# Optimization experiments

Measured on AMD Instinct MI355X. Metric: run time of the kernel, lower is better.

Reference implementation:

```python
import jax, jax.numpy as jnp
import numpy as np

N_NODES = 100000
N_EDGES = 1600000
IN_FEATS = 128
N_HIDDEN = 128
OUT_DIM = 32
BN_EPS = 1e-5


def setup_inputs() -> dict:
    key = jax.random.key(0)
    ks = jax.random.split(key, 12)
    s = 0.05  # weight init scale
    return {
        "features": jax.random.normal(ks[0], (N_NODES, IN_FEATS), dtype=jnp.float32),
        "src": jax.random.randint(ks[1], (N_EDGES,), 0, N_NODES),
        "dst": jax.random.randint(ks[2], (N_EDGES,), 0, N_NODES),
        # layer 0: in_feats -> n_hidden
        "Ws0": jax.random.normal(ks[3], (IN_FEATS, N_HIDDEN), dtype=jnp.float32) * s,
        "Wn0": jax.random.normal(ks[4], (IN_FEATS, N_HIDDEN), dtype=jnp.float32) * s,
        "b0": jnp.zeros((N_HIDDEN,), jnp.float32),
        # layer 1: n_hidden -> n_hidden
        "Ws1": jax.random.normal(ks[5], (N_HIDDEN, N_HIDDEN), dtype=jnp.float32) * s,
        "Wn1": jax.random.normal(ks[6], (N_HIDDEN, N_HIDDEN), dtype=jnp.float32) * s,
        "b1": jnp.zeros((N_HIDDEN,), jnp.float32),
        # layer 2 (output): n_hidden -> out_dim, no activation
        "Ws2": jax.random.normal(ks[7], (N_HIDDEN, OUT_DIM), dtype=jnp.float32) * s,
        "Wn2": jax.random.normal(ks[8], (N_HIDDEN, OUT_DIM), dtype=jnp.float32) * s,
        "b2": jnp.zeros((OUT_DIM,), jnp.float32),
        # batch norms after layers 0 and 1
        "g0": jnp.ones((N_HIDDEN,), jnp.float32),
        "be0": jnp.zeros((N_HIDDEN,), jnp.float32),
        "g1": jnp.ones((N_HIDDEN,), jnp.float32),
        "be1": jnp.zeros((N_HIDDEN,), jnp.float32),
    }


def _sage_mean(h, src, dst, inv_deg, Ws, Wn, b):
    # DGL SAGEConv('mean'): fc_self(h) + fc_neigh(mean of in-neighbor feats)
    agg = jax.ops.segment_sum(h[src], dst, num_segments=N_NODES) * inv_deg
    return h @ Ws + agg @ Wn + b


def _batch_norm(h, gamma, beta):
    mu = jnp.mean(h, axis=0)
    var = jnp.var(h, axis=0)
    return (h - mu) * jax.lax.rsqrt(var + BN_EPS) * gamma + beta


def reference(features, src, dst, Ws0, Wn0, b0, Ws1, Wn1, b1, Ws2, Wn2, b2, g0, be0, g1, be1):
    ones = jnp.ones((N_EDGES,), jnp.float32)
    deg = jax.ops.segment_sum(ones, dst, num_segments=N_NODES)
    inv_deg = (1.0 / jnp.maximum(deg, 1.0))[:, None]  # [N,1]

    # layer 0: SAGEConv internal activation, then BN + external activation
    h = jax.nn.relu(_sage_mean(features, src, dst, inv_deg, Ws0, Wn0, b0))
    h = jax.nn.relu(_batch_norm(h, g0, be0))
    # layer 1 (hidden)
    h = jax.nn.relu(_sage_mean(h, src, dst, inv_deg, Ws1, Wn1, b1))
    h = jax.nn.relu(_batch_norm(h, g1, be1))
    # layer 2 (output): no activation, no BN (idx > n_hidden_layers)
    h = _sage_mean(h, src, dst, inv_deg, Ws2, Wn2, b2)

    # dgl.mean_nodes over a single graph -> [1, out_dim], then softmax over classes
    hg = jnp.mean(h, axis=0, keepdims=True)
    return jax.nn.softmax(hg, axis=1)
```

## Files before the change

kernel.cpp:

```cpp
#include <hip/hip_runtime.h>
#include <hip/hip_bf16.h>

typedef __hip_bfloat16 bf16;
typedef __hip_bfloat162 bf162;

#define NN 100000
#define NE 1600000
#define BN_EPS 1e-5f

#define BSH 8
#define NBUCK ((NN + 255) >> BSH)
#define ABLK 128
#define EPBA ((NE + ABLK - 1) / ABLK)
#define CAP 6144

struct alignas(16) bf16x8 { bf16 v[8]; };

typedef __bf16 bfrag __attribute__((ext_vector_type(8)));
typedef float f4 __attribute__((ext_vector_type(4)));
typedef float f2 __attribute__((ext_vector_type(2)));

static __device__ __forceinline__ float b2f(bf16 x){ return __bfloat162float(x); }
static __device__ __forceinline__ bf16 f2b(float x){ return __float2bfloat16(x); }

static __device__ __forceinline__ uint2 pk8_fp8(float x0,float x1,float x2,float x3,
                                                float x4,float x5,float x6,float x7)
{
    int lo = __builtin_amdgcn_cvt_pk_fp8_f32(x0, x1, 0, 0);
    lo = __builtin_amdgcn_cvt_pk_fp8_f32(x2, x3, lo, 1);
    int hi = __builtin_amdgcn_cvt_pk_fp8_f32(x4, x5, 0, 0);
    hi = __builtin_amdgcn_cvt_pk_fp8_f32(x6, x7, hi, 1);
    return make_uint2((unsigned)lo, (unsigned)hi);
}

__global__ __launch_bounds__(256) void k_convert(const float* __restrict__ in,
                                                 unsigned char* __restrict__ outf8, int n)
{
    int i = (blockIdx.x * 256 + threadIdx.x) * 8;
    if (i + 7 < n) {
        float4 a = *(const float4*)(in + i);
        float4 b = *(const float4*)(in + i + 4);
        *(uint2*)(outf8 + i) = pk8_fp8(a.x,a.y,a.z,a.w,b.x,b.y,b.z,b.w);
    }
}

__global__ __launch_bounds__(256) void k_wtrans(const float* __restrict__ W0, const float* __restrict__ W1,
                                                const float* __restrict__ W2, const float* __restrict__ W3,
                                                bf16* __restrict__ T0, bf16* __restrict__ T1,
                                                bf16* __restrict__ T2, bf16* __restrict__ T3)
{
    int m = blockIdx.x >> 6;
    int t = (blockIdx.x & 63) * 256 + threadIdx.x;
    const float* W = (m == 0) ? W0 : (m == 1) ? W1 : (m == 2) ? W2 : W3;
    bf16* T = (m == 0) ? T0 : (m == 1) ? T1 : (m == 2) ? T2 : T3;
    int n = t >> 7, k = t & 127;
    T[n * 128 + k] = f2b(W[k * 128 + n]);
}

__global__ __launch_bounds__(256) void k_pa1(const int* __restrict__ dst, const int* __restrict__ src,
                                             int* __restrict__ bucketCountD, int* __restrict__ blockBaseD,
                                             int* __restrict__ bucketCountS, int* __restrict__ blockBaseS)
{
    __shared__ int histD[NBUCK];
    __shared__ int histS[NBUCK];
    int t = threadIdx.x;
    for (int i = t; i < NBUCK; i += 256) { histD[i] = 0; histS[i] = 0; }
    __syncthreads();
    int e0 = blockIdx.x * EPBA, e1 = min(e0 + EPBA, NE);
    for (int e = e0 + t; e < e1; e += 256) {
        unsigned bd = ((unsigned)dst[e]) >> BSH;
        unsigned bs = ((unsigned)src[e]) >> BSH;
        if (bd < (unsigned)NBUCK) atomicAdd(&histD[bd], 1);
        if (bs < (unsigned)NBUCK) atomicAdd(&histS[bs], 1);
    }
    __syncthreads();
    for (int i = t; i < NBUCK; i += 256) {
        blockBaseD[blockIdx.x * NBUCK + i] = atomicAdd(&bucketCountD[i], histD[i]);
        blockBaseS[blockIdx.x * NBUCK + i] = atomicAdd(&bucketCountS[i], histS[i]);
    }
}

__global__ __launch_bounds__(512) void k_bscan2(const int* __restrict__ cntD, int* __restrict__ startD,
                                                const int* __restrict__ cntS, int* __restrict__ startS)
{
    __shared__ int sd[512];
    const int* cnt = (blockIdx.x == 0) ? cntD : cntS;
    int* start = (blockIdx.x == 0) ? startD : startS;
    int t = threadIdx.x;
    int v = (t < NBUCK) ? cnt[t] : 0;
    sd[t] = v;
    __syncthreads();
    for (int o = 1; o < 512; o <<= 1) {
        int x = (t >= o) ? sd[t - o] : 0;
        __syncthreads();
        sd[t] += x;
        __syncthreads();
    }
    if (t < NBUCK) start[t] = sd[t] - v;
    if (t == 0) start[NBUCK] = NE;
}

__global__ __launch_bounds__(256) void k_pa2(const int* __restrict__ src, const int* __restrict__ dst,
                                             const int* __restrict__ bucketStartD, const int* __restrict__ blockBaseD,
                                             const int* __restrict__ bucketStartS, const int* __restrict__ blockBaseS,
                                             unsigned* __restrict__ packD, unsigned* __restrict__ packS)
{
    __shared__ int baseD[NBUCK];
    __shared__ int curD[NBUCK];
    __shared__ int baseS[NBUCK];
    __shared__ int curS[NBUCK];
    int t = threadIdx.x;
    for (int i = t; i < NBUCK; i += 256) {
        baseD[i] = bucketStartD[i] + blockBaseD[blockIdx.x * NBUCK + i];
        curD[i] = 0;
        baseS[i] = bucketStartS[i] + blockBaseS[blockIdx.x * NBUCK + i];
        curS[i] = 0;
    }
    __syncthreads();
    int e0 = blockIdx.x * EPBA, e1 = min(e0 + EPBA, NE);
    for (int e = e0 + t; e < e1; e += 256) {
        int s = src[e], d = dst[e];
        unsigned bd = ((unsigned)d) >> BSH;
        if (bd < (unsigned)NBUCK) {
            int r = atomicAdd(&curD[bd], 1);
            unsigned idx = (unsigned)(baseD[bd] + r);
            if (idx < (unsigned)NE)
                packD[idx] = (((unsigned)d & 255u) << 24) | ((unsigned)s & 0xFFFFFFu);
        }
        unsigned bs = ((unsigned)s) >> BSH;
        if (bs < (unsigned)NBUCK) {
            int r = atomicAdd(&curS[bs], 1);
            unsigned idx = (unsigned)(baseS[bs] + r);
            if (idx < (unsigned)NE)
                packS[idx] = (((unsigned)s & 255u) << 24) | ((unsigned)d & 0xFFFFFFu);
        }
    }
}

__global__ __launch_bounds__(256) void k_pbD(const unsigned* __restrict__ packD, const int* __restrict__ bucketStartD,
                                             int* __restrict__ offs, float* __restrict__ invd,
                                             int* __restrict__ esrc)
{
    __shared__ int dcnt[256];
    __shared__ int sscan[256];
    __shared__ int cur[256];
    __shared__ int S[CAP];
    int t = threadIdx.x;
    int b = blockIdx.x;
    int base = b << BSH;
    dcnt[t] = 0;
    cur[t] = 0;
    for (int i = t; i < CAP; i += 256) S[i] = 0;
    __syncthreads();
    int p0 = bucketStartD[b], p1 = bucketStartD[b + 1];
    int cnt = p1 - p0;
    for (int i = p0 + t; i < p1; i += 256)
        atomicAdd(&dcnt[packD[i] >> 24], 1);
    __syncthreads();
    int my = dcnt[t];
    sscan[t] = my;
    __syncthreads();
    for (int o = 1; o < 256; o <<= 1) {
        int v = (t >= o) ? sscan[t - o] : 0;
        __syncthreads();
        sscan[t] += v;
        __syncthreads();
    }
    int lo = sscan[t] - my;
    if (base + t < NN) {
        offs[base + t] = p0 + lo;
        invd[base + t] = 1.0f / (float)max(my, 1);
    }
    if (b == NBUCK - 1 && t == 0) offs[NN] = NE;
    __syncthreads();
    sscan[t] = lo;
    __syncthreads();
    if (cnt <= CAP) {
        for (int i = p0 + t; i < p1; i += 256) {
            unsigned v = packD[i];
            unsigned li = v >> 24;
            int pos = sscan[li] + atomicAdd(&cur[li], 1);
            if ((unsigned)pos >= (unsigned)cnt) pos = cnt - 1;
            S[pos] = (int)(v & 0xFFFFFFu);
        }
        __syncthreads();
        for (int i = t; i < cnt; i += 256) esrc[p0 + i] = S[i];
    } else {
        for (int i = p0 + t; i < p1; i += 256) {
            unsigned v = packD[i];
            unsigned li = v >> 24;
            int pos = sscan[li] + atomicAdd(&cur[li], 1);
            if ((unsigned)pos >= (unsigned)cnt) pos = cnt - 1;
            esrc[p0 + pos] = (int)(v & 0xFFFFFFu);
        }
    }
}

__global__ __launch_bounds__(256) void k_wsrc2(const unsigned* __restrict__ packS, const int* __restrict__ bucketStartS,
                                               const float* __restrict__ invd, float* __restrict__ wsrc)
{
    __shared__ float wacc[256];
    int t = threadIdx.x;
    wacc[t] = 0.f;
    __syncthreads();
    int b = blockIdx.x;
    int base = b << BSH;
    int p0 = bucketStartS[b], p1 = bucketStartS[b + 1];
    for (int i = p0 + t; i < p1; i += 256) {
        unsigned v = packS[i];
        unsigned li = v >> 24;
        unsigned dy = v & 0xFFFFFFu;
        if (dy >= (unsigned)NN) dy = 0u;
        atomicAdd(&wacc[li], invd[dy]);
    }
    __syncthreads();
    if (base + t < NN) wsrc[base + t] = wacc[t];
}

__global__ __launch_bounds__(256) void k_aggregate(const unsigned char* __restrict__ inf8, bf16* __restrict__ out,
                                                   const int* __restrict__ offs, const int* __restrict__ esrc,
                                                   const float* __restrict__ invd,
                                                   const float* __restrict__ scsh, int use_ss)
{
    int row = blockIdx.x * 4 + (threadIdx.x >> 6);
    if (row >= NN) return;
    int lane = threadIdx.x & 63;
    int grp = lane >> 4;
    int c0 = (lane & 15) * 8;
    float sc[8], sh[8];
    if (use_ss) {
#pragma unroll
        for (int j = 0; j < 8; j++) { sc[j] = scsh[c0 + j]; sh[j] = scsh[128 + c0 + j]; }
    }
    int e0 = offs[row], e1 = offs[row + 1];
    float a[8];
#pragma unroll
    for (int j = 0; j < 8; j++) a[j] = 0.f;

    auto unpack = [&](uint2 u, float* v) {
        f2 p0 = __builtin_amdgcn_cvt_pk_f32_fp8(u.x, 0);
        f2 p1 = __builtin_amdgcn_cvt_pk_f32_fp8(u.x, 1);
        f2 p2 = __builtin_amdgcn_cvt_pk_f32_fp8(u.y, 0);
        f2 p3 = __builtin_amdgcn_cvt_pk_f32_fp8(u.y, 1);
        v[0]=p0.x; v[1]=p0.y; v[2]=p1.x; v[3]=p1.y; v[4]=p2.x; v[5]=p2.y; v[6]=p3.x; v[7]=p3.y;
    };

    int e = e0 + grp;
    for (; e + 12 < e1; e += 16) {
        int s0 = esrc[e], s1 = esrc[e + 4], s2 = esrc[e + 8], s3 = esrc[e + 12];
        uint2 u0 = *(const uint2*)&inf8[(size_t)s0 * 128 + c0];
        uint2 u1 = *(const uint2*)&inf8[(size_t)s1 * 128 + c0];
        uint2 u2 = *(const uint2*)&inf8[(size_t)s2 * 128 + c0];
        uint2 u3 = *(const uint2*)&inf8[(size_t)s3 * 128 + c0];
        float v0[8], v1[8], v2[8], v3[8];
        unpack(u0, v0); unpack(u1, v1); unpack(u2, v2); unpack(u3, v3);
        if (use_ss) {
#pragma unroll
            for (int j = 0; j < 8; j++)
                a[j] += fmaxf(v0[j] * sc[j] + sh[j], 0.f) + fmaxf(v1[j] * sc[j] + sh[j], 0.f)
                      + fmaxf(v2[j] * sc[j] + sh[j], 0.f) + fmaxf(v3[j] * sc[j] + sh[j], 0.f);
        } else {
#pragma unroll
            for (int j = 0; j < 8; j++)
                a[j] += (v0[j] + v1[j]) + (v2[j] + v3[j]);
        }
    }
    if (e < e1) {
        int i1 = e + 4, i2 = e + 8;
        float m1 = (i1 < e1) ? 1.f : 0.f;
        float m2 = (i2 < e1) ? 1.f : 0.f;
        if (i1 >= e1) i1 = e;
        if (i2 >= e1) i2 = e;
        int s0 = esrc[e], s1 = esrc[i1], s2 = esrc[i2];
        uint2 u0 = *(const uint2*)&inf8[(size_t)s0 * 128 + c0];
        uint2 u1 = *(const uint2*)&inf8[(size_t)s1 * 128 + c0];
        uint2 u2 = *(const uint2*)&inf8[(size_t)s2 * 128 + c0];
        float v0[8], v1[8], v2[8];
        unpack(u0, v0); unpack(u1, v1); unpack(u2, v2);
        if (use_ss) {
#pragma unroll
            for (int j = 0; j < 8; j++)
                a[j] += fmaxf(v0[j] * sc[j] + sh[j], 0.f)
                      + m1 * fmaxf(v1[j] * sc[j] + sh[j], 0.f)
                      + m2 * fmaxf(v2[j] * sc[j] + sh[j], 0.f);
        } else {
#pragma unroll
            for (int j = 0; j < 8; j++)
                a[j] += v0[j] + m1 * v1[j] + m2 * v2[j];
        }
    }
#pragma unroll
    for (int j = 0; j < 8; j++) {
        a[j] += __shfl_xor(a[j], 16);
        a[j] += __shfl_xor(a[j], 32);
    }
    if (grp == 0) {
        float id = invd[row];
        bf16x8 o;
#pragma unroll
        for (int j = 0; j < 8; j++) o.v[j] = f2b(a[j] * id);
        *(bf16x8*)&out[(size_t)row * 128 + c0] = o;
    }
}

#define GM 64
__global__ __launch_bounds__(256, 4) void k_gemm_mfma(const void* __restrict__ HsSrc, int hs_fp8,
                                                      const bf16* __restrict__ Ag,
                                                      const bf16* __restrict__ Wst, const bf16* __restrict__ Wnt,
                                                      const float* __restrict__ bias,
                                                      const float* __restrict__ scsh, int use_ss,
                                                      bf16* __restrict__ outp, unsigned char* __restrict__ outf8,
                                                      float* __restrict__ bnsums)
{
    __shared__ bf16 sout[64][136];
    __shared__ float sredsum[128], sredsq[128];
    int t = threadIdx.x;
    int lane = t & 63;
    int l16 = lane & 15;
    int quad = lane >> 4;
    int m0 = (t >> 6) * 16;
    int row0 = blockIdx.x * GM;

    if (t < 128) { sredsum[t] = 0.f; sredsq[t] = 0.f; }
    __syncthreads();

    int arow = row0 + m0 + l16;
    int gc = (arow < NN) ? arow : 0;

    bfrag ah[4], aa[4];
#pragma unroll
    for (int ks = 0; ks < 4; ks++)
        aa[ks] = *(const bfrag*)&Ag[(size_t)gc * 128 + ks * 32 + quad * 8];

    if (hs_fp8) {
#pragma unroll
        for (int ks = 0; ks < 4; ks++) {
            int k0 = ks * 32 + quad * 8;
            uint2 u = *(const uint2*)((const unsigned char*)HsSrc + (size_t)gc * 128 + k0);
            f2 q0 = __builtin_amdgcn_cvt_pk_f32_fp8(u.x, 0);
            f2 q1 = __builtin_amdgcn_cvt_pk_f32_fp8(u.x, 1);
            f2 q2 = __builtin_amdgcn_cvt_pk_f32_fp8(u.y, 0);
            f2 q3 = __builtin_amdgcn_cvt_pk_f32_fp8(u.y, 1);
            float hv[8] = {q0.x,q0.y,q1.x,q1.y,q2.x,q2.y,q3.x,q3.y};
            if (use_ss) {
                float4 s0 = *(const float4*)&scsh[k0];
                float4 s1 = *(const float4*)&scsh[k0 + 4];
                float4 h0 = *(const float4*)&scsh[128 + k0];
                float4 h1 = *(const float4*)&scsh[128 + k0 + 4];
                hv[0] = fmaxf(hv[0]*s0.x + h0.x, 0.f); hv[1] = fmaxf(hv[1]*s0.y + h0.y, 0.f);
                hv[2] = fmaxf(hv[2]*s0.z + h0.z, 0.f); hv[3] = fmaxf(hv[3]*s0.w + h0.w, 0.f);
                hv[4] = fmaxf(hv[4]*s1.x + h1.x, 0.f); hv[5] = fmaxf(hv[5]*s1.y + h1.y, 0.f);
                hv[6] = fmaxf(hv[6]*s1.z + h1.z, 0.f); hv[7] = fmaxf(hv[7]*s1.w + h1.w, 0.f);
            }
            bfrag f;
#pragma unroll
            for (int j = 0; j < 8; j++) f[j] = (__bf16)hv[j];
            ah[ks] = f;
        }
    } else {
#pragma unroll
        for (int ks = 0; ks < 4; ks++) {
            int k0 = ks * 32 + quad * 8;
            const float* fp = (const float*)HsSrc + (size_t)gc * 128 + k0;
            float4 x = *(const float4*)fp;
            float4 y = *(const float4*)(fp + 4);
            float hv[8] = {x.x,x.y,x.z,x.w,y.x,y.y,y.z,y.w};
            if (use_ss) {
                float4 s0 = *(const float4*)&scsh[k0];
                float4 s1 = *(const float4*)&scsh[k0 + 4];
                float4 h0 = *(const float4*)&scsh[128 + k0];
                float4 h1 = *(const float4*)&scsh[128 + k0 + 4];
                hv[0] = fmaxf(hv[0]*s0.x + h0.x, 0.f); hv[1] = fmaxf(hv[1]*s0.y + h0.y, 0.f);
                hv[2] = fmaxf(hv[2]*s0.z + h0.z, 0.f); hv[3] = fmaxf(hv[3]*s0.w + h0.w, 0.f);
                hv[4] = fmaxf(hv[4]*s1.x + h1.x, 0.f); hv[5] = fmaxf(hv[5]*s1.y + h1.y, 0.f);
                hv[6] = fmaxf(hv[6]*s1.z + h1.z, 0.f); hv[7] = fmaxf(hv[7]*s1.w + h1.w, 0.f);
            }
            bfrag f;
#pragma unroll
            for (int j = 0; j < 8; j++) f[j] = (__bf16)hv[j];
            ah[ks] = f;
        }
    }

    f4 acc[8];
#pragma unroll
    for (int ct = 0; ct < 8; ct++) { f4 z = {0.f, 0.f, 0.f, 0.f}; acc[ct] = z; }

#pragma unroll
    for (int ks = 0; ks < 4; ks++) {
        int kg = ks * 32 + quad * 8;
#pragma unroll
        for (int ct = 0; ct < 8; ct++) {
            bfrag bs  = *(const bfrag*)&Wst[(ct * 16 + l16) * 128 + kg];
            bfrag bnf = *(const bfrag*)&Wnt[(ct * 16 + l16) * 128 + kg];
            acc[ct] = __builtin_amdgcn_mfma_f32_16x16x32_bf16(ah[ks], bs,  acc[ct], 0, 0, 0);
            acc[ct] = __builtin_amdgcn_mfma_f32_16x16x32_bf16(aa[ks], bnf, acc[ct], 0, 0, 0);
        }
    }

    float psum[8], psq[8];
#pragma unroll
    for (int ct = 0; ct < 8; ct++) {
        float bv = bias[ct * 16 + l16];
        float s = 0.f, s2 = 0.f;
#pragma unroll
        for (int r = 0; r < 4; r++) {
            int lrow = m0 + quad * 4 + r;
            float v = fmaxf(acc[ct][r] + bv, 0.f);
            sout[lrow][ct * 16 + l16] = f2b(v);
            if (row0 + lrow < NN) { s += v; s2 += v * v; }
        }
        psum[ct] = s; psq[ct] = s2;
    }
#pragma unroll
    for (int ct = 0; ct < 8; ct++) {
        psum[ct] += __shfl_xor(psum[ct], 16); psum[ct] += __shfl_xor(psum[ct], 32);
        psq[ct]  += __shfl_xor(psq[ct], 16);  psq[ct]  += __shfl_xor(psq[ct], 32);
    }
    if (lane < 16) {
#pragma unroll
        for (int ct = 0; ct < 8; ct++) {
            atomicAdd(&sredsum[ct * 16 + lane], psum[ct]);
            atomicAdd(&sredsq[ct * 16 + lane],  psq[ct]);
        }
    }

#pragma unroll
    for (int i = 0; i < 4; i++) {
        int idx = i * 64 + lane;
        int row = m0 + (idx >> 4);
        int c16 = idx & 15;
        int grow = row0 + row;
        if (grow < NN) {
            bf16x8 ov = *(const bf16x8*)&sout[row][c16 * 8];
            if (outp) *(bf16x8*)&outp[(size_t)grow * 128 + c16 * 8] = ov;
            if (outf8) {
                *(uint2*)&outf8[(size_t)grow * 128 + c16 * 8] =
                    pk8_fp8(b2f(ov.v[0]), b2f(ov.v[1]), b2f(ov.v[2]), b2f(ov.v[3]),
                            b2f(ov.v[4]), b2f(ov.v[5]), b2f(ov.v[6]), b2f(ov.v[7]));
            }
        }
    }

    __syncthreads();
    if (t < 128) {
        atomicAdd(&bnsums[t], sredsum[t]);
        atomicAdd(&bnsums[128 + t], sredsq[t]);
    }
}

__global__ void k_bn_fin(const float* __restrict__ sums, const float* __restrict__ g,
                         const float* __restrict__ be, float* __restrict__ scsh)
{
    int t = threadIdx.x;
    if (t < 128) {
        float mu = sums[t] / (float)NN;
        float var = sums[128 + t] / (float)NN - mu * mu;
        float sc = g[t] * rsqrtf(var + BN_EPS);
        scsh[t] = sc;
        scsh[128 + t] = be[t] - mu * sc;
    }
}

__global__ __launch_bounds__(256) void k_l2_reduce(const bf16* __restrict__ h, const float* __restrict__ scsh,
                                                   const float* __restrict__ wsrc, float* __restrict__ ue)
{
    __shared__ float su[128], se[128];
    int t = threadIdx.x;
    if (t < 128) { su[t] = 0.f; se[t] = 0.f; }
    __syncthreads();
    int c0 = (t & 15) * 8;
    int rof = t >> 4;
    float sc[8], sh[8];
#pragma unroll
    for (int j = 0; j < 8; j++) { sc[j] = scsh[c0 + j]; sh[j] = scsh[128 + c0 + j]; }
    float u[8], es[8];
#pragma unroll
    for (int j = 0; j < 8; j++) { u[j] = 0.f; es[j] = 0.f; }
    int rpb = (NN + gridDim.x - 1) / gridDim.x;
    int r0 = blockIdx.x * rpb;
    int r1 = min(r0 + rpb, NN);
    for (int r = r0 + rof; r < r1; r += 16) {
        bf16x8 v = *(const bf16x8*)&h[(size_t)r * 128 + c0];
        float w = wsrc[r];
#pragma unroll
        for (int j = 0; j < 8; j++) {
            float x = fmaxf(b2f(v.v[j]) * sc[j] + sh[j], 0.f);
            u[j] += x; es[j] += w * x;
        }
    }
#pragma unroll
    for (int j = 0; j < 8; j++) { atomicAdd(&su[c0 + j], u[j]); atomicAdd(&se[c0 + j], es[j]); }
    __syncthreads();
    if (t < 128) { atomicAdd(&ue[t], su[t]); atomicAdd(&ue[128 + t], se[t]); }
}

__global__ void k_final(const float* __restrict__ ue, const float* __restrict__ Ws2,
                        const float* __restrict__ Wn2, const float* __restrict__ b2,
                        float* __restrict__ out)
{
    __shared__ float logit[32];
    int t = threadIdx.x;
    const float inv = 1.0f / (float)NN;
    if (t < 32) {
        float acc = b2[t];
        for (int k = 0; k < 128; k++)
            acc += (ue[k] * inv) * Ws2[k * 32 + t] + (ue[128 + k] * inv) * Wn2[k * 32 + t];
        logit[t] = acc;
    }
    __syncthreads();
    if (t < 32) {
        float m = -1e30f;
        for (int j = 0; j < 32; j++) m = fmaxf(m, logit[j]);
        float s = 0.f;
        for (int j = 0; j < 32; j++) s += expf(logit[j] - m);
        out[t] = expf(logit[t] - m) / s;
    }
}

extern "C" void kernel_launch(void* const* d_in, const int* in_sizes, int n_in,
                              void* d_out, int out_size, void* d_ws, size_t ws_size,
                              hipStream_t stream)
{
    const float* feat = (const float*)d_in[0];
    const int*   src  = (const int*)d_in[1];
    const int*   dst  = (const int*)d_in[2];
    const float* Ws0  = (const float*)d_in[3];
    const float* Wn0  = (const float*)d_in[4];
    const float* b0   = (const float*)d_in[5];
    const float* Ws1  = (const float*)d_in[6];
    const float* Wn1  = (const float*)d_in[7];
    const float* b1   = (const float*)d_in[8];
    const float* Ws2  = (const float*)d_in[9];
    const float* Wn2  = (const float*)d_in[10];
    const float* b2   = (const float*)d_in[11];
    const float* g0   = (const float*)d_in[12];
    const float* be0  = (const float*)d_in[13];
    const float* g1   = (const float*)d_in[14];
    const float* be1  = (const float*)d_in[15];

    char* p = (char*)d_ws;
    auto alloc = [&](size_t b) -> void* {
        void* r = (void*)p;
        p += (b + 255) & ~(size_t)255;
        return r;
    };
    bf16* A      = (bf16*)alloc((size_t)NN * 128 * 2);
    unsigned char* F8 = (unsigned char*)alloc((size_t)NN * 128);
    unsigned* packS = (unsigned*)alloc((size_t)NE * 4);
    int*  esrc   = (int*)alloc((size_t)NE * 4);
    int*  offs   = (int*)alloc((size_t)(NN + 1) * 4);
    float* invd  = (float*)alloc((size_t)NN * 4);
    float* wsrc  = (float*)alloc((size_t)NN * 4);
    char* zstart = p;
    int*  bucketCountD = (int*)alloc((NBUCK + 1) * 4);
    int*  bucketCountS = (int*)alloc((NBUCK + 1) * 4);
    float* bn0   = (float*)alloc(256 * 4);
    float* bn1   = (float*)alloc(256 * 4);
    float* ue    = (float*)alloc(256 * 4);
    size_t zlen = (size_t)(p - zstart);
    float* scsh0 = (float*)alloc(256 * 4);
    float* scsh1 = (float*)alloc(256 * 4);
    bf16* Ws0t   = (bf16*)alloc(16384 * 2);
    bf16* Wn0t   = (bf16*)alloc(16384 * 2);
    bf16* Ws1t   = (bf16*)alloc(16384 * 2);
    bf16* Wn1t   = (bf16*)alloc(16384 * 2);
    int*  bucketStartD = (int*)alloc((NBUCK + 1) * 4);
    int*  bucketStartS = (int*)alloc((NBUCK + 1) * 4);
    int*  blockBaseD   = (int*)alloc((size_t)ABLK * NBUCK * 4);
    int*  blockBaseS   = (int*)alloc((size_t)ABLK * NBUCK * 4);

    unsigned* packD = (unsigned*)A;

    hipMemsetAsync(zstart, 0, zlen, stream);

    const int GB = (NN + GM - 1) / GM;

    k_convert<<<(NN * 128) / (256 * 8), 256, 0, stream>>>(feat, F8, NN * 128);
    k_wtrans<<<256, 256, 0, stream>>>(Ws0, Wn0, Ws1, Wn1, Ws0t, Wn0t, Ws1t, Wn1t);

    k_pa1<<<ABLK, 256, 0, stream>>>(dst, src, bucketCountD, blockBaseD, bucketCountS, blockBaseS);
    k_bscan2<<<2, 512, 0, stream>>>(bucketCountD, bucketStartD, bucketCountS, bucketStartS);
    k_pa2<<<ABLK, 256, 0, stream>>>(src, dst, bucketStartD, blockBaseD, bucketStartS, blockBaseS, packD, packS);
    k_pbD<<<NBUCK, 256, 0, stream>>>(packD, bucketStartD, offs, invd, esrc);
    k_wsrc2<<<NBUCK, 256, 0, stream>>>(packS, bucketStartS, invd, wsrc);

    k_aggregate<<<(NN + 3) / 4, 256, 0, stream>>>(F8, A, offs, esrc, invd, nullptr, 0);
    k_gemm_mfma<<<GB, 256, 0, stream>>>(feat, 0, A, Ws0t, Wn0t, b0, nullptr, 0, nullptr, F8, bn0);
    k_bn_fin<<<1, 128, 0, stream>>>(bn0, g0, be0, scsh0);

    k_aggregate<<<(NN + 3) / 4, 256, 0, stream>>>(F8, A, offs, esrc, invd, scsh0, 1);
    k_gemm_mfma<<<GB, 256, 0, stream>>>(F8, 1, A, Ws1t, Wn1t, b1, scsh0, 1, A, nullptr, bn1);
    k_bn_fin<<<1, 128, 0, stream>>>(bn1, g1, be1, scsh1);

    k_l2_reduce<<<256, 256, 0, stream>>>(A, scsh1, wsrc, ue);
    k_final<<<1, 64, 0, stream>>>(ue, Ws2, Wn2, b2, (float*)d_out);
}
```

Before: 512.9 us.

## Switch node GEMM to 32x32x16 MFMA with 128-row tiles

Rewrites the fused SAGE GEMM kernel to use 32x32x16 bf16 MFMA instructions, with each wave covering 32 rows, so a block now handles 128 rows instead of 64. Weight fragment loads are amortized over twice as many rows, and the A operands are loaded per k-step inside the loop instead of all up front, which lowers register pressure. The larger shared output tile and the 16-register accumulators raise LDS and VGPR use, which may reduce occupancy, and there are half as many blocks.

Result: faster. 477.3 us (-6.9%).

```diff
diff --git a/kernel.cpp b/kernel.cpp
--- a/kernel.cpp
+++ b/kernel.cpp
@@ -18,6 +18,7 @@
 
 typedef __bf16 bfrag __attribute__((ext_vector_type(8)));
 typedef float f4 __attribute__((ext_vector_type(4)));
+typedef float f16v __attribute__((ext_vector_type(16)));
 typedef float f2 __attribute__((ext_vector_type(2)));
 
 static __device__ __forceinline__ float b2f(bf16 x){ return __bfloat162float(x); }
@@ -303,7 +304,7 @@
     }
 }
 
-#define GM 64
+#define GM 128
 __global__ __launch_bounds__(256, 4) void k_gemm_mfma(const void* __restrict__ HsSrc, int hs_fp8,
                                                       const bf16* __restrict__ Ag,
                                                       const bf16* __restrict__ Wst, const bf16* __restrict__ Wnt,
@@ -312,36 +313,50 @@
                                                       bf16* __restrict__ outp, unsigned char* __restrict__ outf8,
                                                       float* __restrict__ bnsums)
 {
-    __shared__ bf16 sout[64][136];
+    __shared__ bf16 sout[128][136];
     __shared__ float sredsum[128], sredsq[128];
     int t = threadIdx.x;
     int lane = t & 63;
-    int l16 = lane & 15;
-    int quad = lane >> 4;
-    int m0 = (t >> 6) * 16;
+    int l31 = lane & 31;
+    int half = lane >> 5;
+    int m0 = (t >> 6) * 32;
     int row0 = blockIdx.x * GM;
 
     if (t < 128) { sredsum[t] = 0.f; sredsq[t] = 0.f; }
     __syncthreads();
 
-    int arow = row0 + m0 + l16;
+    int arow = row0 + m0 + l31;
     int gc = (arow < NN) ? arow : 0;
 
-    bfrag ah[4], aa[4];
-#pragma unroll
-    for (int ks = 0; ks < 4; ks++)
-        aa[ks] = *(const bfrag*)&Ag[(size_t)gc * 128 + ks * 32 + quad * 8];
-
-    if (hs_fp8) {
-#pragma unroll
-        for (int ks = 0; ks < 4; ks++) {
-            int k0 = ks * 32 + quad * 8;
-            uint2 u = *(const uint2*)((const unsigned char*)HsSrc + (size_t)gc * 128 + k0);
-            f2 q0 = __builtin_amdgcn_cvt_pk_f32_fp8(u.x, 0);
-            f2 q1 = __builtin_amdgcn_cvt_pk_f32_fp8(u.x, 1);
-            f2 q2 = __builtin_amdgcn_cvt_pk_f32_fp8(u.y, 0);
-            f2 q3 = __builtin_amdgcn_cvt_pk_f32_fp8(u.y, 1);
-            float hv[8] = {q0.x,q0.y,q1.x,q1.y,q2.x,q2.y,q3.x,q3.y};
+    f16v acc[4];
+#pragma unroll
+    for (int ct = 0; ct < 4; ct++)
+#pragma unroll
+        for (int r = 0; r < 16; r++) acc[ct][r] = 0.f;
+
+#pragma unroll
+    for (int ks = 0; ks < 8; ks++) {
+        int k0 = ks * 16 + half * 8;
+
+        bfrag aa = *(const bfrag*)&Ag[(size_t)gc * 128 + k0];
+        bfrag ah;
+        {
+            float hv[8];
+            if (hs_fp8) {
+                uint2 u = *(const uint2*)((const unsigned char*)HsSrc + (size_t)gc * 128 + k0);
+                f2 q0 = __builtin_amdgcn_cvt_pk_f32_fp8(u.x, 0);
+                f2 q1 = __builtin_amdgcn_cvt_pk_f32_fp8(u.x, 1);
+                f2 q2 = __builtin_amdgcn_cvt_pk_f32_fp8(u.y, 0);
+                f2 q3 = __builtin_amdgcn_cvt_pk_f32_fp8(u.y, 1);
+                hv[0]=q0.x; hv[1]=q0.y; hv[2]=q1.x; hv[3]=q1.y;
+                hv[4]=q2.x; hv[5]=q2.y; hv[6]=q3.x; hv[7]=q3.y;
+            } else {
+                const float* fp = (const float*)HsSrc + (size_t)gc * 128 + k0;
+                float4 x = *(const float4*)fp;
+                float4 y = *(const float4*)(fp + 4);
+                hv[0]=x.x; hv[1]=x.y; hv[2]=x.z; hv[3]=x.w;
+                hv[4]=y.x; hv[5]=y.y; hv[6]=y.z; hv[7]=y.w;
+            }
             if (use_ss) {
                 float4 s0 = *(const float4*)&scsh[k0];
                 float4 s1 = *(const float4*)&scsh[k0 + 4];
@@ -352,81 +367,49 @@
                 hv[4] = fmaxf(hv[4]*s1.x + h1.x, 0.f); hv[5] = fmaxf(hv[5]*s1.y + h1.y, 0.f);
                 hv[6] = fmaxf(hv[6]*s1.z + h1.z, 0.f); hv[7] = fmaxf(hv[7]*s1.w + h1.w, 0.f);
             }
-            bfrag f;
-#pragma unroll
-            for (int j = 0; j < 8; j++) f[j] = (__bf16)hv[j];
-            ah[ks] = f;
-        }
-    } else {
-#pragma unroll
-        for (int ks = 0; ks < 4; ks++) {
-            int k0 = ks * 32 + quad * 8;
-            const float* fp = (const float*)HsSrc + (size_t)gc * 128 + k0;
-            float4 x = *(const float4*)fp;
-            float4 y = *(const float4*)(fp + 4);
-            float hv[8] = {x.x,x.y,x.z,x.w,y.x,y.y,y.z,y.w};
-            if (use_ss) {
-                float4 s0 = *(const float4*)&scsh[k0];
-                float4 s1 = *(const float4*)&scsh[k0 + 4];
-                float4 h0 = *(const float4*)&scsh[128 + k0];
-                float4 h1 = *(const float4*)&scsh[128 + k0 + 4];
-                hv[0] = fmaxf(hv[0]*s0.x + h0.x, 0.f); hv[1] = fmaxf(hv[1]*s0.y + h0.y, 0.f);
-                hv[2] = fmaxf(hv[2]*s0.z + h0.z, 0.f); hv[3] = fmaxf(hv[3]*s0.w + h0.w, 0.f);
-                hv[4] = fmaxf(hv[4]*s1.x + h1.x, 0.f); hv[5] = fmaxf(hv[5]*s1.y + h1.y, 0.f);
-                hv[6] = fmaxf(hv[6]*s1.z + h1.z, 0.f); hv[7] = fmaxf(hv[7]*s1.w + h1.w, 0.f);
-            }
-            bfrag f;
-#pragma unroll
-            for (int j = 0; j < 8; j++) f[j] = (__bf16)hv[j];
-            ah[ks] = f;
-        }
-    }
-
-    f4 acc[8];
-#pragma unroll
-    for (int ct = 0; ct < 8; ct++) { f4 z = {0.f, 0.f, 0.f, 0.f}; acc[ct] = z; }
-
-#pragma unroll
-    for (int ks = 0; ks < 4; ks++) {
-        int kg = ks * 32 + quad * 8;
-#pragma unroll
-        for (int ct = 0; ct < 8; ct++) {
-            bfrag bs  = *(const bfrag*)&Wst[(ct * 16 + l16) * 128 + kg];
-            bfrag bnf = *(const bfrag*)&Wnt[(ct * 16 + l16) * 128 + kg];
-            acc[ct] = __builtin_amdgcn_mfma_f32_16x16x32_bf16(ah[ks], bs,  acc[ct], 0, 0, 0);
-            acc[ct] = __builtin_amdgcn_mfma_f32_16x16x32_bf16(aa[ks], bnf, acc[ct], 0, 0, 0);
-        }
-    }
-
-    float psum[8], psq[8];
-#pragma unroll
-    for (int ct = 0; ct < 8; ct++) {
-        float bv = bias[ct * 16 + l16];
+#pragma unroll
+            for (int j = 0; j < 8; j++) ah[j] = (__bf16)hv[j];
+        }
+
+#pragma unroll
+        for (int ct = 0; ct < 4; ct++) {
+            bfrag bs  = *(const bfrag*)&Wst[(size_t)(ct * 32 + l31) * 128 + k0];
+            bfrag bnf = *(const bfrag*)&Wnt[(size_t)(ct * 32 + l31) * 128 + k0];
+            acc[ct] = __builtin_amdgcn_mfma_f32_32x32x16_bf16(ah, bs,  acc[ct], 0, 0, 0);
+            acc[ct] = __builtin_amdgcn_mfma_f32_32x32x16_bf16(aa, bnf, acc[ct], 0, 0, 0);
+        }
+    }
+
+    float psum[4], psq[4];
+#pragma unroll
+    for (int ct = 0; ct < 4; ct++) {
+        int col = ct * 32 + l31;
+        float bv = bias[col];
         float s = 0.f, s2 = 0.f;
 #pragma unroll
-        for (int r = 0; r < 4; r++) {
-            int lrow = m0 + quad * 4 + r;
+        for (int r = 0; r < 16; r++) {
+            int lrow = m0 + 4 * half + (r & 3) + 8 * (r >> 2);
             float v = fmaxf(acc[ct][r] + bv, 0.f);
-            sout[lrow][ct * 16 + l16] = f2b(v);
+            sout[lrow][col] = f2b(v);
             if (row0 + lrow < NN) { s += v; s2 += v * v; }
         }
         psum[ct] = s; psq[ct] = s2;
     }
 #pragma unroll
-    for (int ct = 0; ct < 8; ct++) {
-        psum[ct] += __shfl_xor(psum[ct], 16); psum[ct] += __shfl_xor(psum[ct], 32);
-        psq[ct]  += __shfl_xor(psq[ct], 16);  psq[ct]  += __shfl_xor(psq[ct], 32);
-    }
-    if (lane < 16) {
-#pragma unroll
-        for (int ct = 0; ct < 8; ct++) {
-            atomicAdd(&sredsum[ct * 16 + lane], psum[ct]);
-            atomicAdd(&sredsq[ct * 16 + lane],  psq[ct]);
-        }
-    }
-
-#pragma unroll
-    for (int i = 0; i < 4; i++) {
+    for (int ct = 0; ct < 4; ct++) {
+        psum[ct] += __shfl_xor(psum[ct], 32);
+        psq[ct]  += __shfl_xor(psq[ct], 32);
+    }
+    if (lane < 32) {
+#pragma unroll
+        for (int ct = 0; ct < 4; ct++) {
+            atomicAdd(&sredsum[ct * 32 + lane], psum[ct]);
+            atomicAdd(&sredsq[ct * 32 + lane],  psq[ct]);
+        }
+    }
+
+#pragma unroll
+    for (int i = 0; i < 8; i++) {
         int idx = i * 64 + lane;
         int row = m0 + (idx >> 4);
         int c16 = idx & 15;
```
